# Kernel tuning notes

Hardware: AMD Instinct MI355X
Metric: run time of the kernel (lower is better)

The kernel has to match this reference:

```python
import jax, jax.numpy as jnp
import numpy as np

N = 500_000
K = 16
E = N * K
H = 256


def _linear_params(key, fan_in, fan_out):
    k1, k2 = jax.random.split(key)
    bound = 1.0 / np.sqrt(fan_in)
    W = jax.random.uniform(k1, (fan_in, fan_out), jnp.float32, -bound, bound)
    b = jax.random.uniform(k2, (fan_out,), jnp.float32, -bound, bound)
    return W, b


def setup_inputs() -> dict:
    key = jax.random.key(0)
    ks = jax.random.split(key, 10)
    x = jax.random.normal(ks[0], (N, 3), jnp.float32)
    edge_index = jax.random.randint(ks[1], (2, E), 0, N, jnp.int64)
    edge_attr = jax.random.normal(ks[2], (E, 1), jnp.float32)
    W1, b1 = _linear_params(ks[3], K, H)          # GNN1 message MLP: Linear(k, 256)
    We1, be1 = _linear_params(ks[4], H, 128)      # encoder Linear(256,128)
    We2, be2 = _linear_params(ks[5], 128, 6)      # encoder Linear(128,6)
    Wd1, bd1 = _linear_params(ks[6], 6, 128)      # decoder Linear(6,128)
    Wd2, bd2 = _linear_params(ks[7], 128, H)      # decoder Linear(128,256)
    Wo, bo = _linear_params(ks[8], H, 1)          # output Linear(256,1)
    return {"x": x, "edge_index": edge_index, "edge_attr": edge_attr,
            "W1": W1, "b1": b1, "We1": We1, "be1": be1, "We2": We2, "be2": be2,
            "Wd1": Wd1, "bd1": bd1, "Wd2": Wd2, "bd2": bd2, "Wo": Wo, "bo": bo}


def reference(x, edge_index, edge_attr, W1, b1, We1, be1, We2, be2,
              Wd1, bd1, Wd2, bd2, Wo, bo):
    # GNN1: messages are edge_attr verbatim (x_i/x_j ignored); aggregate reshapes
    # all E scalar messages into (N, k) (k edges per node, contiguous) and runs
    # Linear(k,256)+Tanh. Note: LSTM and GCN4 branches in the torch code are dead
    # (GNN1 ignores its node-feature input), so they do not affect the output.
    k = W1.shape[0]
    msgs = edge_attr.reshape(-1, k)                    # (N, k)
    h = jnp.tanh(msgs @ W1 + b1)                       # (N, 256)
    # second L1 call produces the identical result (depends only on edge_attr)
    z = jnp.tanh(jnp.tanh(h @ We1 + be1) @ We2 + be2)  # encoder -> (N, 6)
    d = jnp.tanh(z @ Wd1 + bd1) @ Wd2 + bd2            # decoder -> (N, 256)
    out = jax.nn.sigmoid(jnp.tanh(d) @ Wo + bo)        # (N, 1)
    return out[:, 0]                                   # squeeze(dim=1) -> (N,)
```

## Files before the change

### kernel.cpp

```cpp
#include <hip/hip_runtime.h>


#define N_NODES 500000

#define OFF_W1 0
#define OFF_W2 8192
#define OFF_W3 73728
#define OFF_W4 77824
#define OFF_W5 86016
#define OFF_WO 151552
#define OFF_B1 152576
#define OFF_B2 153600
#define OFF_B3 154112
#define OFF_B4 154176
#define OFF_B5 154688
#define OFF_EXTRA 155712
#define OFF_ZERO  155728
#define IMG_END   156240
#define IMG_ALLOC 156672

#define LDS_SZ IMG_ALLOC

#define SCONST (-2.8853900817779268f)

typedef _Float16 half8  __attribute__((ext_vector_type(8)));
typedef __fp16   pk16x2 __attribute__((ext_vector_type(2)));
typedef float    f32x4  __attribute__((ext_vector_type(4)));
typedef int      int4v  __attribute__((ext_vector_type(4)));

__device__ __align__(16) char g_img[IMG_ALLOC];

static __device__ __forceinline__ unsigned pack_f16_rne(float a, float b) {
  _Float16 ha = (_Float16)a, hb = (_Float16)b;
  unsigned short ua = __builtin_bit_cast(unsigned short, ha);
  unsigned short ub = __builtin_bit_cast(unsigned short, hb);
  return (unsigned)ua | ((unsigned)ub << 16);
}
static __device__ __forceinline__ int pkrtz(float a, float b) {
  pk16x2 h = __builtin_amdgcn_cvt_pkrtz(a, b);
  return __builtin_bit_cast(int, h);
}
static __device__ __forceinline__ float sig2(float y) {
  float e = __builtin_amdgcn_exp2f(y);
  return __builtin_amdgcn_rcpf(1.0f + e);
}
static __device__ __forceinline__ float sigmoid_f(float x) {
  float e = __builtin_amdgcn_exp2f(x * -1.4426950408889634f);
  return __builtin_amdgcn_rcpf(1.0f + e);
}
static __device__ __forceinline__ f32x4 mfma16(half8 a, int4v b, f32x4 c) {
  return __builtin_amdgcn_mfma_f32_16x16x32_f16(a, __builtin_bit_cast(half8, b), c, 0, 0, 0);
}
static __device__ __forceinline__ half8 lda(const char* smem, int off) {
  return *(const half8*)(smem + off);
}
static __device__ __forceinline__ f32x4 ldf4(const char* smem, int off) {
  return *(const f32x4*)(smem + off);
}
#define FENCE() __builtin_amdgcn_sched_barrier(0)

struct PK2 { int lo, hi; };
static __device__ __forceinline__ PK2 tp(f32x4 a) {
  PK2 p;
  p.lo = pkrtz(sig2(a.x), sig2(a.y));
  p.hi = pkrtz(sig2(a.z), sig2(a.w));
  return p;
}

__global__ void gnn_prep(const float* __restrict__ W1,  const float* __restrict__ b1,
                         const float* __restrict__ We1, const float* __restrict__ be1,
                         const float* __restrict__ We2, const float* __restrict__ be2,
                         const float* __restrict__ Wd1, const float* __restrict__ bd1,
                         const float* __restrict__ Wd2, const float* __restrict__ bd2,
                         const float* __restrict__ Wo,  const float* __restrict__ bo)
{
  int t = blockIdx.x * 256 + threadIdx.x;
  int off = t * 4;
  if (off >= IMG_END) return;
  unsigned val;
  if (off < OFF_W2) {
    int rel = off;
    int mi = rel >> 9, li = (rel >> 4) & 31, j2 = (rel >> 2) & 3;
    int fout = mi * 16 + (li & 15);
    int k0 = (li >> 4) * 8 + j2 * 2;
    val = pack_f16_rne(SCONST * W1[k0 * 256 + fout], SCONST * W1[(k0 + 1) * 256 + fout]);
  } else if (off < OFF_W3) {
    int rel = off - OFF_W2;
    int blk = rel >> 10, li = (rel >> 4) & 63, j2 = (rel >> 2) & 3;
    int mi = blk >> 3, ki = blk & 7;
    int fout = mi * 16 + (li & 15);
    int k0 = ki * 32 + 4 * (li >> 4) + 16 * (j2 >> 1) + 2 * (j2 & 1);
    val = pack_f16_rne(2.0f * SCONST * We1[k0 * 128 + fout],
                       2.0f * SCONST * We1[(k0 + 1) * 128 + fout]);
  } else if (off < OFF_W4) {
    int rel = off - OFF_W3;
    int ki = rel >> 10, li = (rel >> 4) & 63, j2 = (rel >> 2) & 3;
    int fo = li & 15;
    int k0 = ki * 32 + 4 * (li >> 4) + 16 * (j2 >> 1) + 2 * (j2 & 1);
    float a = (fo < 6) ? 2.0f * SCONST * We2[k0 * 6 + fo] : 0.0f;
    float b = (fo < 6) ? 2.0f * SCONST * We2[(k0 + 1) * 6 + fo] : 0.0f;
    val = pack_f16_rne(a, b);
  } else if (off < OFF_W5) {
    int rel = off - OFF_W4;
    int mi = rel >> 10, li = (rel >> 4) & 63, j2 = (rel >> 2) & 3;
    int fout = mi * 16 + (li & 15);
    int qa = li >> 4;
    unsigned v = 0;
    if (j2 < 2) {
      int k0 = 4 * qa + 2 * j2;
      float a = (k0 < 6)     ? 2.0f * SCONST * Wd1[k0 * 128 + fout]       : 0.0f;
      float b = (k0 + 1 < 6) ? 2.0f * SCONST * Wd1[(k0 + 1) * 128 + fout] : 0.0f;
      v = pack_f16_rne(a, b);
    }
    val = v;
  } else if (off < OFF_WO) {
    int rel = off - OFF_W5;
    int blk = rel >> 10, li = (rel >> 4) & 63, j2 = (rel >> 2) & 3;
    int mi = blk >> 2, ki = blk & 3;
    int fout = mi * 16 + (li & 15);
    int k0 = ki * 32 + 4 * (li >> 4) + 16 * (j2 >> 1) + 2 * (j2 & 1);
    val = pack_f16_rne(2.0f * SCONST * Wd2[k0 * 256 + fout],
                       2.0f * SCONST * Wd2[(k0 + 1) * 256 + fout]);
  } else if (off < OFF_B1) {
    val = __builtin_bit_cast(unsigned, 2.0f * Wo[(off - OFF_WO) >> 2]);
  } else if (off < OFF_B2) {
    val = __builtin_bit_cast(unsigned, SCONST * b1[(off - OFF_B1) >> 2]);
  } else if (off < OFF_B3) {
    int i = (off - OFF_B2) >> 2;
    float s = 0.0f;
    for (int k = 0; k < 256; ++k) s += We1[k * 128 + i];
    val = __builtin_bit_cast(unsigned, SCONST * (be1[i] - s));
  } else if (off < OFF_B4) {
    int i = (off - OFF_B3) >> 2;
    float v = 0.0f;
    if (i < 6) {
      float s = 0.0f;
      for (int k = 0; k < 128; ++k) s += We2[k * 6 + i];
      v = SCONST * (be2[i] - s);
    }
    val = __builtin_bit_cast(unsigned, v);
  } else if (off < OFF_B5) {
    int i = (off - OFF_B4) >> 2;
    float s = 0.0f;
    for (int k = 0; k < 6; ++k) s += Wd1[k * 128 + i];
    val = __builtin_bit_cast(unsigned, SCONST * (bd1[i] - s));
  } else if (off < OFF_EXTRA) {
    int i = (off - OFF_B5) >> 2;
    float s = 0.0f;
    for (int k = 0; k < 128; ++k) s += Wd2[k * 256 + i];
    val = __builtin_bit_cast(unsigned, SCONST * (bd2[i] - s));
  } else if (off == OFF_EXTRA) {
    float s = 0.0f;
    for (int k = 0; k < 256; ++k) s += Wo[k];
    val = __builtin_bit_cast(unsigned, bo[0] - s);
  } else {
    val = 0;
  }
  *(unsigned*)(g_img + off) = val;
}

static __device__ __forceinline__ void stage_chunk(const char* src, char* dst) {
  __builtin_amdgcn_global_load_lds(
      (const __attribute__((address_space(1))) void*)src,
      (__attribute__((address_space(3))) void*)dst, 16, 0, 0);
}

#define L1_PAIR(KO, OUT_G0, OUT_G1) do {                                   \
    half8 Ae = lda(smem, w1b + (2*(KO))*w1s);                              \
    half8 Ao = lda(smem, w1b + (2*(KO)+1)*w1s);                            \
    f32x4 be_ = ldf4(smem, OFF_B1 + (2*(KO))*64 + q*16);                   \
    f32x4 bo_ = ldf4(smem, OFF_B1 + (2*(KO)+1)*64 + q*16);                 \
    f32x4 ae0 = mfma16(Ae, b1g0, be_);                                     \
    f32x4 ae1 = mfma16(Ae, b1g1, be_);                                     \
    f32x4 ao0 = mfma16(Ao, b1g0, bo_);                                     \
    f32x4 ao1 = mfma16(Ao, b1g1, bo_);                                     \
    PK2 pe0 = tp(ae0), po0 = tp(ao0), pe1 = tp(ae1), po1 = tp(ao1);        \
    OUT_G0.x = pe0.lo; OUT_G0.y = pe0.hi; OUT_G0.z = po0.lo; OUT_G0.w = po0.hi; \
    OUT_G1.x = pe1.lo; OUT_G1.y = pe1.hi; OUT_G1.z = po1.lo; OUT_G1.w = po1.hi; \
    FENCE();                                                               \
  } while (0)

#define L2_MI(MI, ACC0, ACC1) do {                                                            \
    f32x4 bb = ldf4(smem, OFF_B2 + (MI)*64 + q*16);                                           \
    ACC0 = bb; ACC1 = bb;                                                                     \
    half8 A;                                                                                  \
    A = lda(smem, OFF_W2 + ((MI)*8+0)*1024 + ln*16); ACC0 = mfma16(A, c2g0_0, ACC0); ACC1 = mfma16(A, c2g1_0, ACC1); \
    A = lda(smem, OFF_W2 + ((MI)*8+1)*1024 + ln*16); ACC0 = mfma16(A, c2g0_1, ACC0); ACC1 = mfma16(A, c2g1_1, ACC1); \
    A = lda(smem, OFF_W2 + ((MI)*8+2)*1024 + ln*16); ACC0 = mfma16(A, c2g0_2, ACC0); ACC1 = mfma16(A, c2g1_2, ACC1); \
    A = lda(smem, OFF_W2 + ((MI)*8+3)*1024 + ln*16); ACC0 = mfma16(A, c2g0_3, ACC0); ACC1 = mfma16(A, c2g1_3, ACC1); \
    A = lda(smem, OFF_W2 + ((MI)*8+4)*1024 + ln*16); ACC0 = mfma16(A, c2g0_4, ACC0); ACC1 = mfma16(A, c2g1_4, ACC1); \
    A = lda(smem, OFF_W2 + ((MI)*8+5)*1024 + ln*16); ACC0 = mfma16(A, c2g0_5, ACC0); ACC1 = mfma16(A, c2g1_5, ACC1); \
    A = lda(smem, OFF_W2 + ((MI)*8+6)*1024 + ln*16); ACC0 = mfma16(A, c2g0_6, ACC0); ACC1 = mfma16(A, c2g1_6, ACC1); \
    A = lda(smem, OFF_W2 + ((MI)*8+7)*1024 + ln*16); ACC0 = mfma16(A, c2g0_7, ACC0); ACC1 = mfma16(A, c2g1_7, ACC1); \
  } while (0)

#define L2_PAIR(KO, OUT_G0, OUT_G1) do {                                   \
    f32x4 ve0, ve1, vo0, vo1;                                              \
    L2_MI(2*(KO),   ve0, ve1);                                             \
    FENCE();                                                               \
    L2_MI(2*(KO)+1, vo0, vo1);                                             \
    PK2 pe0 = tp(ve0), po0 = tp(vo0), pe1 = tp(ve1), po1 = tp(vo1);        \
    OUT_G0.x = pe0.lo; OUT_G0.y = pe0.hi; OUT_G0.z = po0.lo; OUT_G0.w = po0.hi; \
    OUT_G1.x = pe1.lo; OUT_G1.y = pe1.hi; OUT_G1.z = po1.lo; OUT_G1.w = po1.hi; \
    FENCE();                                                               \
  } while (0)

#define L4_MI(MI, ACC0, ACC1) do {                                         \
    f32x4 bb = ldf4(smem, OFF_B4 + (MI)*64 + q*16);                        \
    half8 A = lda(smem, OFF_W4 + (MI)*1024 + ln*16);                       \
    ACC0 = mfma16(A, b4g0, bb);                                            \
    ACC1 = mfma16(A, b4g1, bb);                                            \
  } while (0)

#define L4_PAIR(KO, OUT_G0, OUT_G1) do {                                   \
    f32x4 ve0, ve1, vo0, vo1;                                              \
    L4_MI(2*(KO),   ve0, ve1);                                             \
    L4_MI(2*(KO)+1, vo0, vo1);                                             \
    PK2 pe0 = tp(ve0), po0 = tp(vo0), pe1 = tp(ve1), po1 = tp(vo1);        \
    OUT_G0.x = pe0.lo; OUT_G0.y = pe0.hi; OUT_G0.z = po0.lo; OUT_G0.w = po0.hi; \
    OUT_G1.x = pe1.lo; OUT_G1.y = pe1.hi; OUT_G1.z = po1.lo; OUT_G1.w = po1.hi; \
    FENCE();                                                               \
  } while (0)

#define L5_MI(MI) do {                                                                        \
    f32x4 bb = ldf4(smem, OFF_B5 + (MI)*64 + q*16);                                           \
    f32x4 a0 = bb, a1 = bb;                                                                   \
    half8 A;                                                                                  \
    A = lda(smem, OFF_W5 + ((MI)*4+0)*1024 + ln*16); a0 = mfma16(A, c5g0_0, a0); a1 = mfma16(A, c5g1_0, a1); \
    A = lda(smem, OFF_W5 + ((MI)*4+1)*1024 + ln*16); a0 = mfma16(A, c5g0_1, a0); a1 = mfma16(A, c5g1_1, a1); \
    A = lda(smem, OFF_W5 + ((MI)*4+2)*1024 + ln*16); a0 = mfma16(A, c5g0_2, a0); a1 = mfma16(A, c5g1_2, a1); \
    A = lda(smem, OFF_W5 + ((MI)*4+3)*1024 + ln*16); a0 = mfma16(A, c5g0_3, a0); a1 = mfma16(A, c5g1_3, a1); \
    f32x4 wo = ldf4(smem, OFF_WO + (MI)*64 + q*16);                                           \
    part0 += sig2(a0.x)*wo.x + sig2(a0.y)*wo.y + sig2(a0.z)*wo.z + sig2(a0.w)*wo.w;           \
    part1 += sig2(a1.x)*wo.x + sig2(a1.y)*wo.y + sig2(a1.z)*wo.z + sig2(a1.w)*wo.w;           \
    FENCE();                                                                                  \
  } while (0)

__global__ __launch_bounds__(512)
void gnn_fused(const float* __restrict__ ea, float* __restrict__ out)
{
  __shared__ __align__(16) char smem[LDS_SZ];
  const int tid = threadIdx.x;
  const int wv = tid >> 6, ln = tid & 63;

#pragma unroll 1
  for (int r = 0; r < 20; ++r) {
    int cb = (r * 8 + wv) << 6;
    if (cb < 9765) {
      stage_chunk(g_img + (size_t)cb * 16 + ln * 16,
                  smem + (size_t)cb * 16 + ln * 16);
    }
  }
  __syncthreads();

  const int q = ln >> 4, c = ln & 15;
  const bool qlo = (q < 2);
  const int lnl16 = (ln & 31) * 16;
  const int w1b = qlo ? (OFF_W1 + lnl16) : (OFF_ZERO + lnl16);
  const int w1s = qlo ? 512 : 0;
  const float bo2 = *(const float*)(smem + OFF_EXTRA);

  const int NG = N_NODES / 32;
  const int g0i = blockIdx.x * 8 + wv;
  const int gstep = gridDim.x << 3;
#pragma unroll 1
  for (int g = g0i; g < NG; g += gstep) {
    const int base = g * 32;

    int nl = base + (q >> 1) * 16 + c;
    if (nl > N_NODES - 1) nl = N_NODES - 1;
    const f32x4* ea4 = (const f32x4*)ea;
    size_t eb = (size_t)nl * 4 + (size_t)((q & 1) * 2);
    f32x4 vlo = ea4[eb];
    f32x4 vhi = ea4[eb + 1];
    int4v b1g0;
    b1g0.x = pkrtz(vlo.x, vlo.y); b1g0.y = pkrtz(vlo.z, vlo.w);
    b1g0.z = pkrtz(vhi.x, vhi.y); b1g0.w = pkrtz(vhi.z, vhi.w);
    int sh = (ln + 32) & 63;
    int4v b1g1;
    b1g1.x = __shfl(b1g0.x, sh, 64); b1g1.y = __shfl(b1g0.y, sh, 64);
    b1g1.z = __shfl(b1g0.z, sh, 64); b1g1.w = __shfl(b1g0.w, sh, 64);

    int4v c2g0_0, c2g0_1, c2g0_2, c2g0_3, c2g0_4, c2g0_5, c2g0_6, c2g0_7;
    int4v c2g1_0, c2g1_1, c2g1_2, c2g1_3, c2g1_4, c2g1_5, c2g1_6, c2g1_7;
    L1_PAIR(0, c2g0_0, c2g1_0);
    L1_PAIR(1, c2g0_1, c2g1_1);
    L1_PAIR(2, c2g0_2, c2g1_2);
    L1_PAIR(3, c2g0_3, c2g1_3);
    L1_PAIR(4, c2g0_4, c2g1_4);
    L1_PAIR(5, c2g0_5, c2g1_5);
    L1_PAIR(6, c2g0_6, c2g1_6);
    L1_PAIR(7, c2g0_7, c2g1_7);

    int4v c3g0_0, c3g0_1, c3g0_2, c3g0_3;
    int4v c3g1_0, c3g1_1, c3g1_2, c3g1_3;
    L2_PAIR(0, c3g0_0, c3g1_0);
    L2_PAIR(1, c3g0_1, c3g1_1);
    L2_PAIR(2, c3g0_2, c3g1_2);
    L2_PAIR(3, c3g0_3, c3g1_3);

    f32x4 bb3 = ldf4(smem, OFF_B3 + q * 16);
    f32x4 z0 = bb3, z1 = bb3;
    half8 A;
    A = lda(smem, OFF_W3 + 0 * 1024 + ln * 16); z0 = mfma16(A, c3g0_0, z0); z1 = mfma16(A, c3g1_0, z1);
    A = lda(smem, OFF_W3 + 1 * 1024 + ln * 16); z0 = mfma16(A, c3g0_1, z0); z1 = mfma16(A, c3g1_1, z1);
    A = lda(smem, OFF_W3 + 2 * 1024 + ln * 16); z0 = mfma16(A, c3g0_2, z0); z1 = mfma16(A, c3g1_2, z1);
    A = lda(smem, OFF_W3 + 3 * 1024 + ln * 16); z0 = mfma16(A, c3g0_3, z0); z1 = mfma16(A, c3g1_3, z1);
    PK2 p3g0 = tp(z0);
    PK2 p3g1 = tp(z1);
    FENCE();

    int4v b4g0, b4g1;
    b4g0.x = p3g0.lo; b4g0.y = p3g0.hi; b4g0.z = 0; b4g0.w = 0;
    b4g1.x = p3g1.lo; b4g1.y = p3g1.hi; b4g1.z = 0; b4g1.w = 0;

    int4v c5g0_0, c5g0_1, c5g0_2, c5g0_3;
    int4v c5g1_0, c5g1_1, c5g1_2, c5g1_3;
    L4_PAIR(0, c5g0_0, c5g1_0);
    L4_PAIR(1, c5g0_1, c5g1_1);
    L4_PAIR(2, c5g0_2, c5g1_2);
    L4_PAIR(3, c5g0_3, c5g1_3);

    float part0 = 0.0f, part1 = 0.0f;
    L5_MI(0);  L5_MI(1);  L5_MI(2);  L5_MI(3);
    L5_MI(4);  L5_MI(5);  L5_MI(6);  L5_MI(7);
    L5_MI(8);  L5_MI(9);  L5_MI(10); L5_MI(11);
    L5_MI(12); L5_MI(13); L5_MI(14); L5_MI(15);

    part0 += __shfl_xor(part0, 16, 64); part0 += __shfl_xor(part0, 32, 64);
    part1 += __shfl_xor(part1, 16, 64); part1 += __shfl_xor(part1, 32, 64);
    if (q < 2) {
      int node = base + q * 16 + c;
      if (node < N_NODES) {
        float v = ((q == 0) ? part0 : part1) + bo2;
        out[node] = sigmoid_f(v);
      }
    }
  }
}

extern "C" void kernel_launch(void* const* d_in, const int* in_sizes, int n_in,
                              void* d_out, int out_size, void* d_ws, size_t ws_size,
                              hipStream_t stream) {
  (void)in_sizes; (void)n_in; (void)ws_size; (void)out_size; (void)d_ws;
  const float* ea  = (const float*)d_in[2];
  const float* W1  = (const float*)d_in[3];
  const float* b1  = (const float*)d_in[4];
  const float* We1 = (const float*)d_in[5];
  const float* be1 = (const float*)d_in[6];
  const float* We2 = (const float*)d_in[7];
  const float* be2 = (const float*)d_in[8];
  const float* Wd1 = (const float*)d_in[9];
  const float* bd1 = (const float*)d_in[10];
  const float* Wd2 = (const float*)d_in[11];
  const float* bd2 = (const float*)d_in[12];
  const float* Wo  = (const float*)d_in[13];
  const float* bo  = (const float*)d_in[14];

  gnn_prep<<<dim3((IMG_END / 4 + 255) / 256), dim3(256), 0, stream>>>(
      W1, b1, We1, be1, We2, be2, Wd1, bd1, Wd2, bd2, Wo, bo);
  gnn_fused<<<dim3(256), dim3(512), 0, stream>>>(ea, (float*)d_out);
}
```

Measured before the change: 242.9 us.

## Move large weight matrices out of LDS to global loads, raise occupancy

Reorders the weight image so that only the small matrices and biases (about 25 KB) are staged into LDS. The two large matrices (We1 and Wd2 fragments) are now read straight from global memory through L2/L1 inside the MFMA loops. The smaller LDS footprint lets more blocks share a CU, and the grid is doubled to 512 blocks. It also parallelizes the bias-folding reductions in the prep kernel, drops some scheduling fences, and removes the node bounds clamps. This trades LDS bandwidth for cache-served global loads, which may stall the MFMA chains.

Result: slower. 518.2 us (+113.4%).

```diff
diff --git a/kernel.cpp b/kernel.cpp
--- a/kernel.cpp
+++ b/kernel.cpp
@@ -4,22 +4,21 @@
 #define N_NODES 500000
 
 #define OFF_W1 0
-#define OFF_W2 8192
-#define OFF_W3 73728
-#define OFF_W4 77824
-#define OFF_W5 86016
-#define OFF_WO 151552
-#define OFF_B1 152576
-#define OFF_B2 153600
-#define OFF_B3 154112
-#define OFF_B4 154176
-#define OFF_B5 154688
-#define OFF_EXTRA 155712
-#define OFF_ZERO  155728
-#define IMG_END   156240
+#define OFF_W3 8192
+#define OFF_W4 12288
+#define OFF_WO 20480
+#define OFF_B1 21504
+#define OFF_B2 22528
+#define OFF_B3 23040
+#define OFF_B4 23104
+#define OFF_B5 23616
+#define OFF_EXTRA 24640
+#define OFF_ZERO  24656
+#define LDS_SZ    25600
+#define OFF_W2 25600
+#define OFF_W5 91136
+#define IMG_END   156672
 #define IMG_ALLOC 156672
-
-#define LDS_SZ IMG_ALLOC
 
 #define SCONST (-2.8853900817779268f)
 
@@ -53,6 +52,9 @@
 }
 static __device__ __forceinline__ half8 lda(const char* smem, int off) {
   return *(const half8*)(smem + off);
+}
+static __device__ __forceinline__ half8 ldw(int off) {
+  return *(const half8*)(g_img + off);
 }
 static __device__ __forceinline__ f32x4 ldf4(const char* smem, int off) {
   return *(const f32x4*)(smem + off);
@@ -67,31 +69,71 @@
   return p;
 }
 
-__global__ void gnn_prep(const float* __restrict__ W1,  const float* __restrict__ b1,
-                         const float* __restrict__ We1, const float* __restrict__ be1,
-                         const float* __restrict__ We2, const float* __restrict__ be2,
-                         const float* __restrict__ Wd1, const float* __restrict__ bd1,
-                         const float* __restrict__ Wd2, const float* __restrict__ bd2,
-                         const float* __restrict__ Wo,  const float* __restrict__ bo)
+__global__ __launch_bounds__(256)
+void gnn_prep(const float* __restrict__ W1,  const float* __restrict__ b1,
+              const float* __restrict__ We1, const float* __restrict__ be1,
+              const float* __restrict__ We2, const float* __restrict__ be2,
+              const float* __restrict__ Wd1, const float* __restrict__ bd1,
+              const float* __restrict__ Wd2, const float* __restrict__ bd2,
+              const float* __restrict__ Wo,  const float* __restrict__ bo)
 {
-  int t = blockIdx.x * 256 + threadIdx.x;
-  int off = t * 4;
+  __shared__ float sb[832];
+  const int tid = threadIdx.x;
+  const int bx = blockIdx.x;
+
+  if (bx >= 153) {
+    float* gB2 = (float*)(g_img + OFF_B2);
+    float* gB3 = (float*)(g_img + OFF_B3);
+    float* gB4 = (float*)(g_img + OFF_B4);
+    float* gB5 = (float*)(g_img + OFF_B5);
+    if (bx == 153) {
+      int col = tid & 127, part = tid >> 7;
+      float s = 0.0f;
+      for (int r = 0; r < 128; ++r) s += We1[(part * 128 + r) * 128 + col];
+      sb[tid] = s;
+      __syncthreads();
+      if (tid < 128) gB2[tid] = SCONST * (be1[tid] - (sb[tid] + sb[128 + tid]));
+    } else if (bx == 154) {
+      float s = 0.0f;
+      for (int r = 0; r < 128; ++r) s += Wd2[r * 256 + tid];
+      gB5[tid] = SCONST * (bd2[tid] - s);
+    } else {
+      for (int j = tid; j < 768; j += 256) sb[j] = We2[j];
+      if (tid >= 192) {
+        int i = tid - 192;
+        sb[768 + i] = Wo[4 * i] + Wo[4 * i + 1] + Wo[4 * i + 2] + Wo[4 * i + 3];
+      }
+      __syncthreads();
+      if (tid < 6) {
+        float s = 0.0f;
+        for (int k = 0; k < 128; ++k) s += sb[k * 6 + tid];
+        gB3[tid] = SCONST * (be2[tid] - s);
+      } else if (tid < 16) {
+        gB3[tid] = 0.0f;
+      } else if (tid == 16) {
+        float s = 0.0f;
+        for (int i = 0; i < 64; ++i) s += sb[768 + i];
+        *(float*)(g_img + OFF_EXTRA) = bo[0] - s;
+      } else if (tid >= 32 && tid < 160) {
+        int i = tid - 32;
+        float s = 0.0f;
+        for (int k = 0; k < 6; ++k) s += Wd1[k * 128 + i];
+        gB4[i] = SCONST * (bd1[i] - s);
+      }
+    }
+    return;
+  }
+
+  int off = (bx * 256 + tid) * 4;
   if (off >= IMG_END) return;
+  if (off >= OFF_B2 && off < OFF_EXTRA + 4) return;
   unsigned val;
-  if (off < OFF_W2) {
+  if (off < OFF_W3) {
     int rel = off;
     int mi = rel >> 9, li = (rel >> 4) & 31, j2 = (rel >> 2) & 3;
     int fout = mi * 16 + (li & 15);
     int k0 = (li >> 4) * 8 + j2 * 2;
     val = pack_f16_rne(SCONST * W1[k0 * 256 + fout], SCONST * W1[(k0 + 1) * 256 + fout]);
-  } else if (off < OFF_W3) {
-    int rel = off - OFF_W2;
-    int blk = rel >> 10, li = (rel >> 4) & 63, j2 = (rel >> 2) & 3;
-    int mi = blk >> 3, ki = blk & 7;
-    int fout = mi * 16 + (li & 15);
-    int k0 = ki * 32 + 4 * (li >> 4) + 16 * (j2 >> 1) + 2 * (j2 & 1);
-    val = pack_f16_rne(2.0f * SCONST * We1[k0 * 128 + fout],
-                       2.0f * SCONST * We1[(k0 + 1) * 128 + fout]);
   } else if (off < OFF_W4) {
     int rel = off - OFF_W3;
     int ki = rel >> 10, li = (rel >> 4) & 63, j2 = (rel >> 2) & 3;
@@ -100,7 +142,7 @@
     float a = (fo < 6) ? 2.0f * SCONST * We2[k0 * 6 + fo] : 0.0f;
     float b = (fo < 6) ? 2.0f * SCONST * We2[(k0 + 1) * 6 + fo] : 0.0f;
     val = pack_f16_rne(a, b);
-  } else if (off < OFF_W5) {
+  } else if (off < OFF_WO) {
     int rel = off - OFF_W4;
     int mi = rel >> 10, li = (rel >> 4) & 63, j2 = (rel >> 2) & 3;
     int fout = mi * 16 + (li & 15);
@@ -113,7 +155,21 @@
       v = pack_f16_rne(a, b);
     }
     val = v;
-  } else if (off < OFF_WO) {
+  } else if (off < OFF_B1) {
+    val = __builtin_bit_cast(unsigned, 2.0f * Wo[(off - OFF_WO) >> 2]);
+  } else if (off < OFF_B2) {
+    val = __builtin_bit_cast(unsigned, SCONST * b1[(off - OFF_B1) >> 2]);
+  } else if (off < OFF_W2) {
+    val = 0;
+  } else if (off < OFF_W5) {
+    int rel = off - OFF_W2;
+    int blk = rel >> 10, li = (rel >> 4) & 63, j2 = (rel >> 2) & 3;
+    int mi = blk >> 3, ki = blk & 7;
+    int fout = mi * 16 + (li & 15);
+    int k0 = ki * 32 + 4 * (li >> 4) + 16 * (j2 >> 1) + 2 * (j2 & 1);
+    val = pack_f16_rne(2.0f * SCONST * We1[k0 * 128 + fout],
+                       2.0f * SCONST * We1[(k0 + 1) * 128 + fout]);
+  } else {
     int rel = off - OFF_W5;
     int blk = rel >> 10, li = (rel >> 4) & 63, j2 = (rel >> 2) & 3;
     int mi = blk >> 2, ki = blk & 3;
@@ -121,40 +177,6 @@
     int k0 = ki * 32 + 4 * (li >> 4) + 16 * (j2 >> 1) + 2 * (j2 & 1);
     val = pack_f16_rne(2.0f * SCONST * Wd2[k0 * 256 + fout],
                        2.0f * SCONST * Wd2[(k0 + 1) * 256 + fout]);
-  } else if (off < OFF_B1) {
-    val = __builtin_bit_cast(unsigned, 2.0f * Wo[(off - OFF_WO) >> 2]);
-  } else if (off < OFF_B2) {
-    val = __builtin_bit_cast(unsigned, SCONST * b1[(off - OFF_B1) >> 2]);
-  } else if (off < OFF_B3) {
-    int i = (off - OFF_B2) >> 2;
-    float s = 0.0f;
-    for (int k = 0; k < 256; ++k) s += We1[k * 128 + i];
-    val = __builtin_bit_cast(unsigned, SCONST * (be1[i] - s));
-  } else if (off < OFF_B4) {
-    int i = (off - OFF_B3) >> 2;
-    float v = 0.0f;
-    if (i < 6) {
-      float s = 0.0f;
-      for (int k = 0; k < 128; ++k) s += We2[k * 6 + i];
-      v = SCONST * (be2[i] - s);
-    }
-    val = __builtin_bit_cast(unsigned, v);
-  } else if (off < OFF_B5) {
-    int i = (off - OFF_B4) >> 2;
-    float s = 0.0f;
-    for (int k = 0; k < 6; ++k) s += Wd1[k * 128 + i];
-    val = __builtin_bit_cast(unsigned, SCONST * (bd1[i] - s));
-  } else if (off < OFF_EXTRA) {
-    int i = (off - OFF_B5) >> 2;
-    float s = 0.0f;
-    for (int k = 0; k < 128; ++k) s += Wd2[k * 256 + i];
-    val = __builtin_bit_cast(unsigned, SCONST * (bd2[i] - s));
-  } else if (off == OFF_EXTRA) {
-    float s = 0.0f;
-    for (int k = 0; k < 256; ++k) s += Wo[k];
-    val = __builtin_bit_cast(unsigned, bo[0] - s);
-  } else {
-    val = 0;
   }
   *(unsigned*)(g_img + off) = val;
 }
@@ -184,14 +206,14 @@
     f32x4 bb = ldf4(smem, OFF_B2 + (MI)*64 + q*16);                                           \
     ACC0 = bb; ACC1 = bb;                                                                     \
     half8 A;                                                                                  \
-    A = lda(smem, OFF_W2 + ((MI)*8+0)*1024 + ln*16); ACC0 = mfma16(A, c2g0_0, ACC0); ACC1 = mfma16(A, c2g1_0, ACC1); \
-    A = lda(smem, OFF_W2 + ((MI)*8+1)*1024 + ln*16); ACC0 = mfma16(A, c2g0_1, ACC0); ACC1 = mfma16(A, c2g1_1, ACC1); \
-    A = lda(smem, OFF_W2 + ((MI)*8+2)*1024 + ln*16); ACC0 = mfma16(A, c2g0_2, ACC0); ACC1 = mfma16(A, c2g1_2, ACC1); \
-    A = lda(smem, OFF_W2 + ((MI)*8+3)*1024 + ln*16); ACC0 = mfma16(A, c2g0_3, ACC0); ACC1 = mfma16(A, c2g1_3, ACC1); \
-    A = lda(smem, OFF_W2 + ((MI)*8+4)*1024 + ln*16); ACC0 = mfma16(A, c2g0_4, ACC0); ACC1 = mfma16(A, c2g1_4, ACC1); \
-    A = lda(smem, OFF_W2 + ((MI)*8+5)*1024 + ln*16); ACC0 = mfma16(A, c2g0_5, ACC0); ACC1 = mfma16(A, c2g1_5, ACC1); \
-    A = lda(smem, OFF_W2 + ((MI)*8+6)*1024 + ln*16); ACC0 = mfma16(A, c2g0_6, ACC0); ACC1 = mfma16(A, c2g1_6, ACC1); \
-    A = lda(smem, OFF_W2 + ((MI)*8+7)*1024 + ln*16); ACC0 = mfma16(A, c2g0_7, ACC0); ACC1 = mfma16(A, c2g1_7, ACC1); \
+    A = ldw(OFF_W2 + ((MI)*8+0)*1024 + ln16); ACC0 = mfma16(A, c2g0_0, ACC0); ACC1 = mfma16(A, c2g1_0, ACC1); \
+    A = ldw(OFF_W2 + ((MI)*8+1)*1024 + ln16); ACC0 = mfma16(A, c2g0_1, ACC0); ACC1 = mfma16(A, c2g1_1, ACC1); \
+    A = ldw(OFF_W2 + ((MI)*8+2)*1024 + ln16); ACC0 = mfma16(A, c2g0_2, ACC0); ACC1 = mfma16(A, c2g1_2, ACC1); \
+    A = ldw(OFF_W2 + ((MI)*8+3)*1024 + ln16); ACC0 = mfma16(A, c2g0_3, ACC0); ACC1 = mfma16(A, c2g1_3, ACC1); \
+    A = ldw(OFF_W2 + ((MI)*8+4)*1024 + ln16); ACC0 = mfma16(A, c2g0_4, ACC0); ACC1 = mfma16(A, c2g1_4, ACC1); \
+    A = ldw(OFF_W2 + ((MI)*8+5)*1024 + ln16); ACC0 = mfma16(A, c2g0_5, ACC0); ACC1 = mfma16(A, c2g1_5, ACC1); \
+    A = ldw(OFF_W2 + ((MI)*8+6)*1024 + ln16); ACC0 = mfma16(A, c2g0_6, ACC0); ACC1 = mfma16(A, c2g1_6, ACC1); \
+    A = ldw(OFF_W2 + ((MI)*8+7)*1024 + ln16); ACC0 = mfma16(A, c2g0_7, ACC0); ACC1 = mfma16(A, c2g1_7, ACC1); \
   } while (0)
 
 #define L2_PAIR(KO, OUT_G0, OUT_G1) do {                                   \
@@ -207,7 +229,7 @@
 
 #define L4_MI(MI, ACC0, ACC1) do {                                         \
     f32x4 bb = ldf4(smem, OFF_B4 + (MI)*64 + q*16);                        \
-    half8 A = lda(smem, OFF_W4 + (MI)*1024 + ln*16);                       \
+    half8 A = lda(smem, OFF_W4 + (MI)*1024 + ln16);                        \
     ACC0 = mfma16(A, b4g0, bb);                                            \
     ACC1 = mfma16(A, b4g1, bb);                                            \
   } while (0)
@@ -219,21 +241,19 @@
     PK2 pe0 = tp(ve0), po0 = tp(vo0), pe1 = tp(ve1), po1 = tp(vo1);        \
     OUT_G0.x = pe0.lo; OUT_G0.y = pe0.hi; OUT_G0.z = po0.lo; OUT_G0.w = po0.hi; \
     OUT_G1.x = pe1.lo; OUT_G1.y = pe1.hi; OUT_G1.z = po1.lo; OUT_G1.w = po1.hi; \
-    FENCE();                                                               \
   } while (0)
 
 #define L5_MI(MI) do {                                                                        \
     f32x4 bb = ldf4(smem, OFF_B5 + (MI)*64 + q*16);                                           \
     f32x4 a0 = bb, a1 = bb;                                                                   \
     half8 A;                                                                                  \
-    A = lda(smem, OFF_W5 + ((MI)*4+0)*1024 + ln*16); a0 = mfma16(A, c5g0_0, a0); a1 = mfma16(A, c5g1_0, a1); \
-    A = lda(smem, OFF_W5 + ((MI)*4+1)*1024 + ln*16); a0 = mfma16(A, c5g0_1, a0); a1 = mfma16(A, c5g1_1, a1); \
-    A = lda(smem, OFF_W5 + ((MI)*4+2)*1024 + ln*16); a0 = mfma16(A, c5g0_2, a0); a1 = mfma16(A, c5g1_2, a1); \
-    A = lda(smem, OFF_W5 + ((MI)*4+3)*1024 + ln*16); a0 = mfma16(A, c5g0_3, a0); a1 = mfma16(A, c5g1_3, a1); \
+    A = ldw(OFF_W5 + ((MI)*4+0)*1024 + ln16); a0 = mfma16(A, c5g0_0, a0); a1 = mfma16(A, c5g1_0, a1); \
+    A = ldw(OFF_W5 + ((MI)*4+1)*1024 + ln16); a0 = mfma16(A, c5g0_1, a0); a1 = mfma16(A, c5g1_1, a1); \
+    A = ldw(OFF_W5 + ((MI)*4+2)*1024 + ln16); a0 = mfma16(A, c5g0_2, a0); a1 = mfma16(A, c5g1_2, a1); \
+    A = ldw(OFF_W5 + ((MI)*4+3)*1024 + ln16); a0 = mfma16(A, c5g0_3, a0); a1 = mfma16(A, c5g1_3, a1); \
     f32x4 wo = ldf4(smem, OFF_WO + (MI)*64 + q*16);                                           \
     part0 += sig2(a0.x)*wo.x + sig2(a0.y)*wo.y + sig2(a0.z)*wo.z + sig2(a0.w)*wo.w;           \
     part1 += sig2(a1.x)*wo.x + sig2(a1.y)*wo.y + sig2(a1.z)*wo.z + sig2(a1.w)*wo.w;           \
-    FENCE();                                                                                  \
   } while (0)
 
 __global__ __launch_bounds__(512)
@@ -244,9 +264,9 @@
   const int wv = tid >> 6, ln = tid & 63;
 
 #pragma unroll 1
-  for (int r = 0; r < 20; ++r) {
+  for (int r = 0; r < 4; ++r) {
     int cb = (r * 8 + wv) << 6;
-    if (cb < 9765) {
+    if (cb < LDS_SZ / 16) {
       stage_chunk(g_img + (size_t)cb * 16 + ln * 16,
                   smem + (size_t)cb * 16 + ln * 16);
     }
@@ -254,6 +274,7 @@
   __syncthreads();
 
   const int q = ln >> 4, c = ln & 15;
+  const int ln16 = ln * 16;
   const bool qlo = (q < 2);
   const int lnl16 = (ln & 31) * 16;
   const int w1b = qlo ? (OFF_W1 + lnl16) : (OFF_ZERO + lnl16);
@@ -268,7 +289,6 @@
     const int base = g * 32;
 
     int nl = base + (q >> 1) * 16 + c;
-    if (nl > N_NODES - 1) nl = N_NODES - 1;
     const f32x4* ea4 = (const f32x4*)ea;
     size_t eb = (size_t)nl * 4 + (size_t)((q & 1) * 2);
     f32x4 vlo = ea4[eb];
@@ -302,10 +322,10 @@
     f32x4 bb3 = ldf4(smem, OFF_B3 + q * 16);
     f32x4 z0 = bb3, z1 = bb3;
     half8 A;
-    A = lda(smem, OFF_W3 + 0 * 1024 + ln * 16); z0 = mfma16(A, c3g0_0, z0); z1 = mfma16(A, c3g1_0, z1);
-    A = lda(smem, OFF_W3 + 1 * 1024 + ln * 16); z0 = mfma16(A, c3g0_1, z0); z1 = mfma16(A, c3g1_1, z1);
-    A = lda(smem, OFF_W3 + 2 * 1024 + ln * 16); z0 = mfma16(A, c3g0_2, z0); z1 = mfma16(A, c3g1_2, z1);
-    A = lda(smem, OFF_W3 + 3 * 1024 + ln * 16); z0 = mfma16(A, c3g0_3, z0); z1 = mfma16(A, c3g1_3, z1);
+    A = lda(smem, OFF_W3 + 0 * 1024 + ln16); z0 = mfma16(A, c3g0_0, z0); z1 = mfma16(A, c3g1_0, z1);
+    A = lda(smem, OFF_W3 + 1 * 1024 + ln16); z0 = mfma16(A, c3g0_1, z0); z1 = mfma16(A, c3g1_1, z1);
+    A = lda(smem, OFF_W3 + 2 * 1024 + ln16); z0 = mfma16(A, c3g0_2, z0); z1 = mfma16(A, c3g1_2, z1);
+    A = lda(smem, OFF_W3 + 3 * 1024 + ln16); z0 = mfma16(A, c3g0_3, z0); z1 = mfma16(A, c3g1_3, z1);
     PK2 p3g0 = tp(z0);
     PK2 p3g1 = tp(z1);
     FENCE();
@@ -331,10 +351,8 @@
     part1 += __shfl_xor(part1, 16, 64); part1 += __shfl_xor(part1, 32, 64);
     if (q < 2) {
       int node = base + q * 16 + c;
-      if (node < N_NODES) {
-        float v = ((q == 0) ? part0 : part1) + bo2;
-        out[node] = sigmoid_f(v);
-      }
+      float v = ((q == 0) ? part0 : part1) + bo2;
+      out[node] = sigmoid_f(v);
     }
   }
 }
@@ -357,7 +375,7 @@
   const float* Wo  = (const float*)d_in[13];
   const float* bo  = (const float*)d_in[14];
 
-  gnn_prep<<<dim3((IMG_END / 4 + 255) / 256), dim3(256), 0, stream>>>(
+  gnn_prep<<<dim3(156), dim3(256), 0, stream>>>(
       W1, b1, We1, be1, We2, be2, Wd1, bd1, Wd2, bd2, Wo, bo);
-  gnn_fused<<<dim3(256), dim3(512), 0, stream>>>(ea, (float*)d_out);
-}
+  gnn_fused<<<dim3(512), dim3(512), 0, stream>>>(ea, (float*)d_out);
+}
```
